# Kernel tuning notes

Measured on AMD Instinct MI355X. Metric: run time of the kernel, lower is better.

The kernel has to match this reference:

```python
import jax, jax.numpy as jnp
import numpy as np

D_MODEL = 512
SEQ_LEN = 2048
S = 32  # local window size
BATCH = 2


def setup_inputs() -> dict:
    key = jax.random.key(0)
    ks = jax.random.split(key, 12)
    shp = (SEQ_LEN, BATCH, D_MODEL)
    return {
        "query": jax.random.normal(ks[0], shp, jnp.float32),
        "key": jax.random.normal(ks[1], shp, jnp.float32),
        "value": jax.random.normal(ks[2], shp, jnp.float32),
        "Wq": jax.random.normal(ks[3], (D_MODEL, D_MODEL), jnp.float32) * 0.02,
        "bq": jax.random.normal(ks[4], (D_MODEL,), jnp.float32) * 0.01,
        "Wk": jax.random.normal(ks[5], (D_MODEL, D_MODEL), jnp.float32) * 0.02,
        "bk": jax.random.normal(ks[6], (D_MODEL,), jnp.float32) * 0.01,
        "Wv": jax.random.normal(ks[7], (D_MODEL, D_MODEL), jnp.float32) * 0.02,
        "bv": jax.random.normal(ks[8], (D_MODEL,), jnp.float32) * 0.01,
        "pos_bias": jax.random.normal(ks[9], (SEQ_LEN, SEQ_LEN), jnp.float32) * 0.02,
        "Wo": jax.random.normal(ks[10], (D_MODEL, D_MODEL), jnp.float32) * 0.02,
        "bo": jax.random.normal(ks[11], (D_MODEL,), jnp.float32) * 0.01,
    }


def _aft_local(query, key, value, Wq, bq, Wk, bk, Wv, bv, pos_bias, Wo, bo):
    T, B, D = query.shape
    q = query @ Wq.T + bq  # [T,B,D]
    k = key @ Wk.T + bk
    v = value @ Wv.T + bv
    pb = pos_bias[:T, :T]

    # max_logit: elementwise max of per-dim key max and (key + col-max of pos_bias) max,
    # then batch index 0 (faithful to original `[0]` indexing) -> shape [D]
    max_logit = jnp.maximum(k.max(axis=0),
                            (k + pb.max(axis=0)[:, None, None]).max(axis=0))[0]

    # out-of-window running sums: tokens t' <= t - S contribute exp(k) (no pos bias)
    ek = jnp.exp(k - max_logit)                 # [T,B,D]
    cs_num = jnp.cumsum(ek * v, axis=0)
    cs_den = jnp.cumsum(ek, axis=0)
    t_arr = jnp.arange(T)
    prefix_idx = jnp.clip(t_arr - S, 0, T - 1)
    has_prefix = (t_arr >= S)[:, None, None]
    num_out = jnp.where(has_prefix, cs_num[prefix_idx], 0.0)
    den_out = jnp.where(has_prefix, cs_den[prefix_idx], 0.0)

    # in-window part: t' in [max(0, t-S+1), t] with pos_bias[t, t']
    j = jnp.arange(S)
    idx_raw = t_arr[:, None] - S + 1 + j[None, :]   # [T,S]
    valid = (idx_raw >= 0).astype(k.dtype)
    idx = jnp.clip(idx_raw, 0, T - 1)
    k_win = k[idx]                                  # [T,S,B,D]
    v_win = v[idx]                                  # [T,S,B,D]
    pb_win = pb[t_arr[:, None], idx]                # [T,S]
    exp_l = jnp.exp(k_win + pb_win[:, :, None, None] - max_logit) * valid[:, :, None, None]
    num_in = (exp_l * v_win).sum(axis=1)            # [T,B,D]
    den_in = exp_l.sum(axis=1)

    y = jax.nn.sigmoid(q) * (num_out + num_in) / (den_out + den_in)
    return y @ Wo.T + bo


def reference(query, key, value, Wq, bq, Wk, bk, Wv, bv, pos_bias, Wo, bo):
    return _aft_local(query, key, value, Wq, bq, Wk, bk, Wv, bv, pos_bias, Wo, bo)
```

## Files before the change

### kernel.cpp

```cpp
#include <hip/hip_runtime.h>
#include <hip/hip_bf16.h>

#define TT 2048
#define BB 2
#define DD 512
#define BD (BB*DD)
#define SS 32
#define MR (TT*BB)
#define NE (TT*BB*DD)
#define CH 32

typedef __bf16 bf16x8 __attribute__((ext_vector_type(8)));
typedef float f32x4 __attribute__((ext_vector_type(4)));

__device__ __forceinline__ void async_copy16(void* lds, const void* gptr) {
    __builtin_amdgcn_global_load_lds(
        (const __attribute__((address_space(1))) void*)gptr,
        (__attribute__((address_space(3))) void*)lds,
        16, 0, 0);
}

__global__ __launch_bounds__(256) void cast_all(
    const float* __restrict__ s0, const float* __restrict__ s1, const float* __restrict__ s2,
    const float* __restrict__ w0, const float* __restrict__ w1,
    const float* __restrict__ w2, const float* __restrict__ w3,
    __hip_bfloat16* __restrict__ d0, __hip_bfloat16* __restrict__ d1, __hip_bfloat16* __restrict__ d2,
    __hip_bfloat16* __restrict__ e0, __hip_bfloat16* __restrict__ e1,
    __hip_bfloat16* __restrict__ e2, __hip_bfloat16* __restrict__ e3)
{
    int b = blockIdx.x;
    const float* s;
    __hip_bfloat16* d;
    size_t i;
    if (b < 6144) {
        int which = b >> 11;
        s = which == 0 ? s0 : (which == 1 ? s1 : s2);
        d = which == 0 ? d0 : (which == 1 ? d1 : d2);
        i = ((size_t)(b & 2047) * 256 + threadIdx.x) * 4;
    } else {
        int b2 = b - 6144;
        int which = b2 >> 8;
        s = which == 0 ? w0 : (which == 1 ? w1 : (which == 2 ? w2 : w3));
        d = which == 0 ? e0 : (which == 1 ? e1 : (which == 2 ? e2 : e3));
        i = ((size_t)(b2 & 255) * 256 + threadIdx.x) * 4;
    }
    float4 f = *(const float4*)(s + i);
    union { __hip_bfloat16 h[4]; ushort4 u; } cv;
    cv.h[0] = __float2bfloat16(f.x); cv.h[1] = __float2bfloat16(f.y);
    cv.h[2] = __float2bfloat16(f.z); cv.h[3] = __float2bfloat16(f.w);
    *(ushort4*)((unsigned short*)d + i) = cv.u;
}

__global__ __launch_bounds__(256) void gemm_qkv(
    const __hip_bfloat16* __restrict__ qb, const __hip_bfloat16* __restrict__ kb,
    const __hip_bfloat16* __restrict__ vb,
    const __hip_bfloat16* __restrict__ Wqb, const __hip_bfloat16* __restrict__ Wkb,
    const __hip_bfloat16* __restrict__ Wvb,
    const float* __restrict__ bq, const float* __restrict__ bk,
    const float* __restrict__ bv,
    float* __restrict__ qout, float* __restrict__ ek, float* __restrict__ ekv,
    float* __restrict__ part_d, float* __restrict__ part_n)
{
    __shared__ char smem[16384];
    const int tid = threadIdx.x;
    const int lane = tid & 63;
    const int wv = tid >> 6;
    const int wave_m = wv >> 1, wave_n = wv & 1;
    const int m0 = blockIdx.y * 64, n0 = blockIdx.x * 64;
    const int kq = lane >> 4, rr = lane & 15;

    if (blockIdx.z == 0) {
        f32x4 acc[2][2] = {};
        const __hip_bfloat16* Arow = qb + (size_t)(m0 + lane) * DD + wv * 8;
        const __hip_bfloat16* Wrow = Wqb + (size_t)(n0 + lane) * DD + wv * 8;
        char* ldsA = &smem[wv * 1024];
        char* ldsW = &smem[4096 + wv * 1024];
        for (int k0 = 0; k0 < DD; k0 += 32) {
            __syncthreads();
            async_copy16(ldsA, Arow + k0);
            async_copy16(ldsW, Wrow + k0);
            __syncthreads();
            bf16x8 a0 = *(const bf16x8*)&smem[kq*1024 + (wave_m*32 +  0 + rr)*16];
            bf16x8 a1 = *(const bf16x8*)&smem[kq*1024 + (wave_m*32 + 16 + rr)*16];
            bf16x8 b0 = *(const bf16x8*)&smem[4096 + kq*1024 + (wave_n*32 +  0 + rr)*16];
            bf16x8 b1 = *(const bf16x8*)&smem[4096 + kq*1024 + (wave_n*32 + 16 + rr)*16];
            acc[0][0] = __builtin_amdgcn_mfma_f32_16x16x32_bf16(a0, b0, acc[0][0], 0, 0, 0);
            acc[0][1] = __builtin_amdgcn_mfma_f32_16x16x32_bf16(a0, b1, acc[0][1], 0, 0, 0);
            acc[1][0] = __builtin_amdgcn_mfma_f32_16x16x32_bf16(a1, b0, acc[1][0], 0, 0, 0);
            acc[1][1] = __builtin_amdgcn_mfma_f32_16x16x32_bf16(a1, b1, acc[1][1], 0, 0, 0);
        }
        #pragma unroll
        for (int ms = 0; ms < 2; ++ms)
            #pragma unroll
            for (int ns = 0; ns < 2; ++ns) {
                int n = n0 + wave_n*32 + ns*16 + rr;
                float bn = bq[n];
                #pragma unroll
                for (int r = 0; r < 4; ++r) {
                    int m = m0 + wave_m*32 + ms*16 + kq*4 + r;
                    qout[(size_t)m * DD + n] = acc[ms][ns][r] + bn;
                }
            }
    } else {
        f32x4 acck[2][2] = {}, accv[2][2] = {};
        const __hip_bfloat16* AKrow = kb + (size_t)(m0 + lane) * DD + wv * 8;
        const __hip_bfloat16* WKrow = Wkb + (size_t)(n0 + lane) * DD + wv * 8;
        const __hip_bfloat16* AVrow = vb + (size_t)(m0 + lane) * DD + wv * 8;
        const __hip_bfloat16* WVrow = Wvb + (size_t)(n0 + lane) * DD + wv * 8;
        char* ldsAK = &smem[wv * 1024];
        char* ldsWK = &smem[4096 + wv * 1024];
        char* ldsAV = &smem[8192 + wv * 1024];
        char* ldsWV = &smem[12288 + wv * 1024];
        for (int k0 = 0; k0 < DD; k0 += 32) {
            __syncthreads();
            async_copy16(ldsAK, AKrow + k0);
            async_copy16(ldsWK, WKrow + k0);
            async_copy16(ldsAV, AVrow + k0);
            async_copy16(ldsWV, WVrow + k0);
            __syncthreads();
            bf16x8 ak0 = *(const bf16x8*)&smem[kq*1024 + (wave_m*32 +  0 + rr)*16];
            bf16x8 ak1 = *(const bf16x8*)&smem[kq*1024 + (wave_m*32 + 16 + rr)*16];
            bf16x8 bk0 = *(const bf16x8*)&smem[4096 + kq*1024 + (wave_n*32 +  0 + rr)*16];
            bf16x8 bk1 = *(const bf16x8*)&smem[4096 + kq*1024 + (wave_n*32 + 16 + rr)*16];
            bf16x8 av0 = *(const bf16x8*)&smem[8192 + kq*1024 + (wave_m*32 +  0 + rr)*16];
            bf16x8 av1 = *(const bf16x8*)&smem[8192 + kq*1024 + (wave_m*32 + 16 + rr)*16];
            bf16x8 bv0 = *(const bf16x8*)&smem[12288 + kq*1024 + (wave_n*32 +  0 + rr)*16];
            bf16x8 bv1 = *(const bf16x8*)&smem[12288 + kq*1024 + (wave_n*32 + 16 + rr)*16];
            acck[0][0] = __builtin_amdgcn_mfma_f32_16x16x32_bf16(ak0, bk0, acck[0][0], 0, 0, 0);
            acck[0][1] = __builtin_amdgcn_mfma_f32_16x16x32_bf16(ak0, bk1, acck[0][1], 0, 0, 0);
            acck[1][0] = __builtin_amdgcn_mfma_f32_16x16x32_bf16(ak1, bk0, acck[1][0], 0, 0, 0);
            acck[1][1] = __builtin_amdgcn_mfma_f32_16x16x32_bf16(ak1, bk1, acck[1][1], 0, 0, 0);
            accv[0][0] = __builtin_amdgcn_mfma_f32_16x16x32_bf16(av0, bv0, accv[0][0], 0, 0, 0);
            accv[0][1] = __builtin_amdgcn_mfma_f32_16x16x32_bf16(av0, bv1, accv[0][1], 0, 0, 0);
            accv[1][0] = __builtin_amdgcn_mfma_f32_16x16x32_bf16(av1, bv0, accv[1][0], 0, 0, 0);
            accv[1][1] = __builtin_amdgcn_mfma_f32_16x16x32_bf16(av1, bv1, accv[1][1], 0, 0, 0);
        }
        float sd[2][2] = {{0.f,0.f},{0.f,0.f}};
        float sn[2][2] = {{0.f,0.f},{0.f,0.f}};
        #pragma unroll
        for (int ms = 0; ms < 2; ++ms)
            #pragma unroll
            for (int ns = 0; ns < 2; ++ns) {
                int n = n0 + wave_n*32 + ns*16 + rr;
                float bkn = bk[n], bvn = bv[n];
                #pragma unroll
                for (int r = 0; r < 4; ++r) {
                    int m = m0 + wave_m*32 + ms*16 + kq*4 + r;
                    float e  = expf(acck[ms][ns][r] + bkn);
                    float nv = e * (accv[ms][ns][r] + bvn);
                    ek[(size_t)m * DD + n]  = e;
                    ekv[(size_t)m * DD + n] = nv;
                    sd[ns][r & 1] += e;
                    sn[ns][r & 1] += nv;
                }
            }
        #pragma unroll
        for (int ns = 0; ns < 2; ++ns)
            #pragma unroll
            for (int par = 0; par < 2; ++par) {
                sd[ns][par] += __shfl_xor(sd[ns][par], 16, 64);
                sd[ns][par] += __shfl_xor(sd[ns][par], 32, 64);
                sn[ns][par] += __shfl_xor(sn[ns][par], 16, 64);
                sn[ns][par] += __shfl_xor(sn[ns][par], 32, 64);
            }
        __syncthreads();
        float* red = (float*)smem;
        if (lane < 16) {
            #pragma unroll
            for (int ns = 0; ns < 2; ++ns) {
                int c = wave_n*32 + ns*16 + rr;
                red[(0*2 + wave_m)*64 + c] = sd[ns][0];
                red[(1*2 + wave_m)*64 + c] = sd[ns][1];
                red[(2*2 + wave_m)*64 + c] = sn[ns][0];
                red[(3*2 + wave_m)*64 + c] = sn[ns][1];
            }
        }
        __syncthreads();
        {
            int which = tid >> 6;
            int c = tid & 63;
            float s = red[(which*2 + 0)*64 + c] + red[(which*2 + 1)*64 + c];
            int b = which & 1;
            float* dst = (which < 2) ? part_d : part_n;
            dst[(size_t)blockIdx.y * BD + b*512 + n0 + c] = s;
        }
    }
}

__global__ __launch_bounds__(256) void fused_window(
    const float* __restrict__ q, const float* __restrict__ ek,
    const float* __restrict__ ekv, const float* __restrict__ part_d,
    const float* __restrict__ part_n, const float* __restrict__ pb,
    __hip_bfloat16* __restrict__ yb)
{
    __shared__ float wl[CH][SS];
    const int tid = threadIdx.x;
    const int col = blockIdx.x * 256 + tid;
    const int chunk = blockIdx.y;
    const int t0 = chunk * CH;

    #pragma unroll
    for (int i = 0; i < (CH * SS) / 256; ++i) {
        int idx = tid + i * 256;
        int tl = idx >> 5, j = idx & 31;
        int t = t0 + tl;
        int u = t - (SS - 1) + j;
        float w = 0.f;
        if (u >= 0) w = expf(pb[(size_t)t * TT + u]);
        wl[tl][j] = w;
    }
    __syncthreads();

    float ring_d[32], ring_n[32];
    float cs_d = 0.f, cs_n = 0.f;
    const bool hasp = (chunk > 0);
    if (hasp) {
        float pref_d = 0.f, pref_n = 0.f;
        for (int p = 0; p < chunk; ++p) {
            pref_d += part_d[(size_t)p * BD + col];
            pref_n += part_n[(size_t)p * BD + col];
        }
        float ssd = 0.f, ssn = 0.f;
        #pragma unroll
        for (int i = 0; i < 32; ++i) {
            size_t off = (size_t)(t0 - 32 + i) * BD + col;
            float e = ek[off];
            float n = ekv[off];
            ring_d[i] = e; ring_n[i] = n;
            ssd += e; ssn += n;
        }
        cs_d = pref_d - ssd;
        cs_n = pref_n - ssn;
    } else {
        #pragma unroll
        for (int i = 0; i < 32; ++i) { ring_d[i] = 0.f; ring_n[i] = 0.f; }
    }

    #pragma unroll
    for (int s = 0; s < CH; ++s) {
        int t = t0 + s;
        size_t off = (size_t)t * BD + col;
        float e = ek[off];
        float n = ekv[off];
        cs_d += ring_d[s];
        cs_n += ring_n[s];
        ring_d[s] = e;
        ring_n[s] = n;
        float den = 0.f, num = 0.f;
        #pragma unroll
        for (int j4 = 0; j4 < 8; ++j4) {
            float4 w4 = *(const float4*)&wl[s][j4 * 4];
            den += w4.x * ring_d[(s + 1 + j4*4 + 0) & 31];
            num += w4.x * ring_n[(s + 1 + j4*4 + 0) & 31];
            den += w4.y * ring_d[(s + 1 + j4*4 + 1) & 31];
            num += w4.y * ring_n[(s + 1 + j4*4 + 1) & 31];
            den += w4.z * ring_d[(s + 1 + j4*4 + 2) & 31];
            num += w4.z * ring_n[(s + 1 + j4*4 + 2) & 31];
            den += w4.w * ring_d[(s + 1 + j4*4 + 3) & 31];
            num += w4.w * ring_n[(s + 1 + j4*4 + 3) & 31];
        }
        if (hasp) { den += cs_d; num += cs_n; }
        float qv = q[off];
        float sig = 1.f / (1.f + expf(-qv));
        yb[off] = __float2bfloat16(sig * num / den);
    }
}

__global__ __launch_bounds__(256) void gemm_out(
    const __hip_bfloat16* __restrict__ yb, const __hip_bfloat16* __restrict__ Wob,
    const float* __restrict__ bo, float* __restrict__ out)
{
    __shared__ char smem[8192];
    const int tid = threadIdx.x;
    const int lane = tid & 63;
    const int wv = tid >> 6;
    const int wave_m = wv >> 1, wave_n = wv & 1;
    const int m0 = blockIdx.y * 64, n0 = blockIdx.x * 64;
    const int kq = lane >> 4, rr = lane & 15;

    f32x4 acc[2][2] = {};
    const __hip_bfloat16* Arow = yb + (size_t)(m0 + lane) * DD + wv * 8;
    const __hip_bfloat16* Wrow = Wob + (size_t)(n0 + lane) * DD + wv * 8;
    char* ldsA = &smem[wv * 1024];
    char* ldsW = &smem[4096 + wv * 1024];

    for (int k0 = 0; k0 < DD; k0 += 32) {
        __syncthreads();
        async_copy16(ldsA, Arow + k0);
        async_copy16(ldsW, Wrow + k0);
        __syncthreads();
        bf16x8 a0 = *(const bf16x8*)&smem[kq*1024 + (wave_m*32 +  0 + rr)*16];
        bf16x8 a1 = *(const bf16x8*)&smem[kq*1024 + (wave_m*32 + 16 + rr)*16];
        bf16x8 b0 = *(const bf16x8*)&smem[4096 + kq*1024 + (wave_n*32 +  0 + rr)*16];
        bf16x8 b1 = *(const bf16x8*)&smem[4096 + kq*1024 + (wave_n*32 + 16 + rr)*16];
        acc[0][0] = __builtin_amdgcn_mfma_f32_16x16x32_bf16(a0, b0, acc[0][0], 0, 0, 0);
        acc[0][1] = __builtin_amdgcn_mfma_f32_16x16x32_bf16(a0, b1, acc[0][1], 0, 0, 0);
        acc[1][0] = __builtin_amdgcn_mfma_f32_16x16x32_bf16(a1, b0, acc[1][0], 0, 0, 0);
        acc[1][1] = __builtin_amdgcn_mfma_f32_16x16x32_bf16(a1, b1, acc[1][1], 0, 0, 0);
    }
    #pragma unroll
    for (int ms = 0; ms < 2; ++ms)
        #pragma unroll
        for (int ns = 0; ns < 2; ++ns) {
            int n = n0 + wave_n*32 + ns*16 + rr;
            float bn = bo[n];
            #pragma unroll
            for (int r = 0; r < 4; ++r) {
                int m = m0 + wave_m*32 + ms*16 + kq*4 + r;
                out[(size_t)m * DD + n] = acc[ms][ns][r] + bn;
            }
        }
}

extern "C" void kernel_launch(void* const* d_in, const int* in_sizes, int n_in,
                              void* d_out, int out_size, void* d_ws, size_t ws_size,
                              hipStream_t stream) {
    const float* query = (const float*)d_in[0];
    const float* key   = (const float*)d_in[1];
    const float* value = (const float*)d_in[2];
    const float* Wq    = (const float*)d_in[3];
    const float* bq    = (const float*)d_in[4];
    const float* Wk    = (const float*)d_in[5];
    const float* bk    = (const float*)d_in[6];
    const float* Wv    = (const float*)d_in[7];
    const float* bv    = (const float*)d_in[8];
    const float* pb    = (const float*)d_in[9];
    const float* Wo    = (const float*)d_in[10];
    const float* bo    = (const float*)d_in[11];
    float* out = (float*)d_out;

    float* ws = (float*)d_ws;
    float* q      = ws;
    float* ek     = ws + (size_t)NE;
    float* ekv    = ws + (size_t)2 * NE;
    float* part_d = ws + (size_t)3 * NE;
    float* part_n = part_d + 65536;
    __hip_bfloat16* bfb = (__hip_bfloat16*)(part_n + 65536);
    __hip_bfloat16* qb  = bfb;
    __hip_bfloat16* kb  = bfb + (size_t)NE;
    __hip_bfloat16* vb  = bfb + (size_t)2 * NE;
    __hip_bfloat16* yb  = bfb + (size_t)3 * NE;
    __hip_bfloat16* Wqb = bfb + (size_t)4 * NE;
    __hip_bfloat16* Wkb = Wqb + 262144;
    __hip_bfloat16* Wvb = Wkb + 262144;
    __hip_bfloat16* Wob = Wvb + 262144;

    cast_all<<<7168, 256, 0, stream>>>(query, key, value, Wq, Wk, Wv, Wo,
                                       qb, kb, vb, Wqb, Wkb, Wvb, Wob);

    gemm_qkv<<<dim3(DD / 64, MR / 64, 2), 256, 0, stream>>>(
        qb, kb, vb, Wqb, Wkb, Wvb, bq, bk, bv,
        q, ek, ekv, part_d, part_n);

    fused_window<<<dim3(BD / 256, TT / CH), 256, 0, stream>>>(
        q, ek, ekv, part_d, part_n, pb, yb);

    gemm_out<<<dim3(DD / 64, MR / 64), 256, 0, stream>>>(yb, Wob, bo, out);
}
```

Measured before the change: 174.8 us.

## Triple-buffer GEMM K-loops with async LDS prefetch and interleave ek/ekv storage

Replaces the load-then-compute loops in the QKV and output GEMMs with a three-stage LDS ring. Tiles are prefetched two iterations ahead using explicit vmcnt waits and raw barriers, so global-to-LDS copies overlap MFMA work. It also interleaves the ek/ekv outputs and the per-chunk partial sums into float2 pairs, so the window kernel issues one vector load instead of two scalar loads. The prefix-sum loop uses four independent accumulators. LDS use per block grows threefold, which may reduce occupancy, and the hand-written waitcnt logic must count outstanding copies correctly.

```diff
diff --git a/kernel.cpp b/kernel.cpp
--- a/kernel.cpp
+++ b/kernel.cpp
@@ -19,6 +19,8 @@
         (__attribute__((address_space(3))) void*)lds,
         16, 0, 0);
 }
+
+#define MFMA16(a,b,c) __builtin_amdgcn_mfma_f32_16x16x32_bf16((a),(b),(c),0,0,0)
 
 __global__ __launch_bounds__(256) void cast_all(
     const float* __restrict__ s0, const float* __restrict__ s1, const float* __restrict__ s2,
@@ -58,10 +60,10 @@
     const __hip_bfloat16* __restrict__ Wvb,
     const float* __restrict__ bq, const float* __restrict__ bk,
     const float* __restrict__ bv,
-    float* __restrict__ qout, float* __restrict__ ek, float* __restrict__ ekv,
-    float* __restrict__ part_d, float* __restrict__ part_n)
+    float* __restrict__ qout, float* __restrict__ ekn,
+    float* __restrict__ part)
 {
-    __shared__ char smem[16384];
+    __shared__ char smem[49152];
     const int tid = threadIdx.x;
     const int lane = tid & 63;
     const int wv = tid >> 6;
@@ -73,21 +75,33 @@
         f32x4 acc[2][2] = {};
         const __hip_bfloat16* Arow = qb + (size_t)(m0 + lane) * DD + wv * 8;
         const __hip_bfloat16* Wrow = Wqb + (size_t)(n0 + lane) * DD + wv * 8;
-        char* ldsA = &smem[wv * 1024];
-        char* ldsW = &smem[4096 + wv * 1024];
-        for (int k0 = 0; k0 < DD; k0 += 32) {
-            __syncthreads();
-            async_copy16(ldsA, Arow + k0);
-            async_copy16(ldsW, Wrow + k0);
-            __syncthreads();
-            bf16x8 a0 = *(const bf16x8*)&smem[kq*1024 + (wave_m*32 +  0 + rr)*16];
-            bf16x8 a1 = *(const bf16x8*)&smem[kq*1024 + (wave_m*32 + 16 + rr)*16];
-            bf16x8 b0 = *(const bf16x8*)&smem[4096 + kq*1024 + (wave_n*32 +  0 + rr)*16];
-            bf16x8 b1 = *(const bf16x8*)&smem[4096 + kq*1024 + (wave_n*32 + 16 + rr)*16];
-            acc[0][0] = __builtin_amdgcn_mfma_f32_16x16x32_bf16(a0, b0, acc[0][0], 0, 0, 0);
-            acc[0][1] = __builtin_amdgcn_mfma_f32_16x16x32_bf16(a0, b1, acc[0][1], 0, 0, 0);
-            acc[1][0] = __builtin_amdgcn_mfma_f32_16x16x32_bf16(a1, b0, acc[1][0], 0, 0, 0);
-            acc[1][1] = __builtin_amdgcn_mfma_f32_16x16x32_bf16(a1, b1, acc[1][1], 0, 0, 0);
+        async_copy16(smem + 0*8192 +        wv*1024, Arow + 0);
+        async_copy16(smem + 0*8192 + 4096 + wv*1024, Wrow + 0);
+        async_copy16(smem + 1*8192 +        wv*1024, Arow + 32);
+        async_copy16(smem + 1*8192 + 4096 + wv*1024, Wrow + 32);
+        asm volatile("s_waitcnt vmcnt(2)" ::: "memory");
+        __builtin_amdgcn_s_barrier();
+        #pragma unroll
+        for (int it = 0; it < 16; ++it) {
+            if (it + 2 < 16) {
+                char* nb = smem + ((it + 2) % 3) * 8192;
+                async_copy16(nb +        wv*1024, Arow + (it+2)*32);
+                async_copy16(nb + 4096 + wv*1024, Wrow + (it+2)*32);
+            }
+            const char* cb = smem + (it % 3) * 8192;
+            bf16x8 a0 = *(const bf16x8*)(cb + kq*1024 + (wave_m*32 +  0 + rr)*16);
+            bf16x8 a1 = *(const bf16x8*)(cb + kq*1024 + (wave_m*32 + 16 + rr)*16);
+            bf16x8 w0 = *(const bf16x8*)(cb + 4096 + kq*1024 + (wave_n*32 +  0 + rr)*16);
+            bf16x8 w1 = *(const bf16x8*)(cb + 4096 + kq*1024 + (wave_n*32 + 16 + rr)*16);
+            acc[0][0] = MFMA16(a0, w0, acc[0][0]);
+            acc[0][1] = MFMA16(a0, w1, acc[0][1]);
+            acc[1][0] = MFMA16(a1, w0, acc[1][0]);
+            acc[1][1] = MFMA16(a1, w1, acc[1][1]);
+            if (it < 15) {
+                if (it < 14) asm volatile("s_waitcnt vmcnt(2) lgkmcnt(0)" ::: "memory");
+                else         asm volatile("s_waitcnt vmcnt(0) lgkmcnt(0)" ::: "memory");
+                __builtin_amdgcn_s_barrier();
+            }
         }
         #pragma unroll
         for (int ms = 0; ms < 2; ++ms)
@@ -107,33 +121,47 @@
         const __hip_bfloat16* WKrow = Wkb + (size_t)(n0 + lane) * DD + wv * 8;
         const __hip_bfloat16* AVrow = vb + (size_t)(m0 + lane) * DD + wv * 8;
         const __hip_bfloat16* WVrow = Wvb + (size_t)(n0 + lane) * DD + wv * 8;
-        char* ldsAK = &smem[wv * 1024];
-        char* ldsWK = &smem[4096 + wv * 1024];
-        char* ldsAV = &smem[8192 + wv * 1024];
-        char* ldsWV = &smem[12288 + wv * 1024];
-        for (int k0 = 0; k0 < DD; k0 += 32) {
-            __syncthreads();
-            async_copy16(ldsAK, AKrow + k0);
-            async_copy16(ldsWK, WKrow + k0);
-            async_copy16(ldsAV, AVrow + k0);
-            async_copy16(ldsWV, WVrow + k0);
-            __syncthreads();
-            bf16x8 ak0 = *(const bf16x8*)&smem[kq*1024 + (wave_m*32 +  0 + rr)*16];
-            bf16x8 ak1 = *(const bf16x8*)&smem[kq*1024 + (wave_m*32 + 16 + rr)*16];
-            bf16x8 bk0 = *(const bf16x8*)&smem[4096 + kq*1024 + (wave_n*32 +  0 + rr)*16];
-            bf16x8 bk1 = *(const bf16x8*)&smem[4096 + kq*1024 + (wave_n*32 + 16 + rr)*16];
-            bf16x8 av0 = *(const bf16x8*)&smem[8192 + kq*1024 + (wave_m*32 +  0 + rr)*16];
-            bf16x8 av1 = *(const bf16x8*)&smem[8192 + kq*1024 + (wave_m*32 + 16 + rr)*16];
-            bf16x8 bv0 = *(const bf16x8*)&smem[12288 + kq*1024 + (wave_n*32 +  0 + rr)*16];
-            bf16x8 bv1 = *(const bf16x8*)&smem[12288 + kq*1024 + (wave_n*32 + 16 + rr)*16];
-            acck[0][0] = __builtin_amdgcn_mfma_f32_16x16x32_bf16(ak0, bk0, acck[0][0], 0, 0, 0);
-            acck[0][1] = __builtin_amdgcn_mfma_f32_16x16x32_bf16(ak0, bk1, acck[0][1], 0, 0, 0);
-            acck[1][0] = __builtin_amdgcn_mfma_f32_16x16x32_bf16(ak1, bk0, acck[1][0], 0, 0, 0);
-            acck[1][1] = __builtin_amdgcn_mfma_f32_16x16x32_bf16(ak1, bk1, acck[1][1], 0, 0, 0);
-            accv[0][0] = __builtin_amdgcn_mfma_f32_16x16x32_bf16(av0, bv0, accv[0][0], 0, 0, 0);
-            accv[0][1] = __builtin_amdgcn_mfma_f32_16x16x32_bf16(av0, bv1, accv[0][1], 0, 0, 0);
-            accv[1][0] = __builtin_amdgcn_mfma_f32_16x16x32_bf16(av1, bv0, accv[1][0], 0, 0, 0);
-            accv[1][1] = __builtin_amdgcn_mfma_f32_16x16x32_bf16(av1, bv1, accv[1][1], 0, 0, 0);
+        #pragma unroll
+        for (int pt = 0; pt < 2; ++pt) {
+            char* nb = smem + pt * 16384;
+            async_copy16(nb +         wv*1024, AKrow + pt*32);
+            async_copy16(nb +  4096 + wv*1024, WKrow + pt*32);
+            async_copy16(nb +  8192 + wv*1024, AVrow + pt*32);
+            async_copy16(nb + 12288 + wv*1024, WVrow + pt*32);
+        }
+        asm volatile("s_waitcnt vmcnt(4)" ::: "memory");
+        __builtin_amdgcn_s_barrier();
+        #pragma unroll
+        for (int it = 0; it < 16; ++it) {
+            if (it + 2 < 16) {
+                char* nb = smem + ((it + 2) % 3) * 16384;
+                async_copy16(nb +         wv*1024, AKrow + (it+2)*32);
+                async_copy16(nb +  4096 + wv*1024, WKrow + (it+2)*32);
+                async_copy16(nb +  8192 + wv*1024, AVrow + (it+2)*32);
+                async_copy16(nb + 12288 + wv*1024, WVrow + (it+2)*32);
+            }
+            const char* cb = smem + (it % 3) * 16384;
+            bf16x8 ak0 = *(const bf16x8*)(cb +         kq*1024 + (wave_m*32 +  0 + rr)*16);
+            bf16x8 ak1 = *(const bf16x8*)(cb +         kq*1024 + (wave_m*32 + 16 + rr)*16);
+            bf16x8 bk0 = *(const bf16x8*)(cb +  4096 + kq*1024 + (wave_n*32 +  0 + rr)*16);
+            bf16x8 bk1 = *(const bf16x8*)(cb +  4096 + kq*1024 + (wave_n*32 + 16 + rr)*16);
+            bf16x8 av0 = *(const bf16x8*)(cb +  8192 + kq*1024 + (wave_m*32 +  0 + rr)*16);
+            bf16x8 av1 = *(const bf16x8*)(cb +  8192 + kq*1024 + (wave_m*32 + 16 + rr)*16);
+            bf16x8 bv0 = *(const bf16x8*)(cb + 12288 + kq*1024 + (wave_n*32 +  0 + rr)*16);
+            bf16x8 bv1 = *(const bf16x8*)(cb + 12288 + kq*1024 + (wave_n*32 + 16 + rr)*16);
+            acck[0][0] = MFMA16(ak0, bk0, acck[0][0]);
+            acck[0][1] = MFMA16(ak0, bk1, acck[0][1]);
+            acck[1][0] = MFMA16(ak1, bk0, acck[1][0]);
+            acck[1][1] = MFMA16(ak1, bk1, acck[1][1]);
+            accv[0][0] = MFMA16(av0, bv0, accv[0][0]);
+            accv[0][1] = MFMA16(av0, bv1, accv[0][1]);
+            accv[1][0] = MFMA16(av1, bv0, accv[1][0]);
+            accv[1][1] = MFMA16(av1, bv1, accv[1][1]);
+            if (it < 15) {
+                if (it < 14) asm volatile("s_waitcnt vmcnt(4) lgkmcnt(0)" ::: "memory");
+                else         asm volatile("s_waitcnt vmcnt(0) lgkmcnt(0)" ::: "memory");
+                __builtin_amdgcn_s_barrier();
+            }
         }
         float sd[2][2] = {{0.f,0.f},{0.f,0.f}};
         float sn[2][2] = {{0.f,0.f},{0.f,0.f}};
@@ -148,8 +176,8 @@
                     int m = m0 + wave_m*32 + ms*16 + kq*4 + r;
                     float e  = expf(acck[ms][ns][r] + bkn);
                     float nv = e * (accv[ms][ns][r] + bvn);
-                    ek[(size_t)m * DD + n]  = e;
-                    ekv[(size_t)m * DD + n] = nv;
+                    float2 st; st.x = e; st.y = nv;
+                    *(float2*)&ekn[((size_t)m * DD + n) * 2] = st;
                     sd[ns][r & 1] += e;
                     sn[ns][r & 1] += nv;
                 }
@@ -181,16 +209,15 @@
             int c = tid & 63;
             float s = red[(which*2 + 0)*64 + c] + red[(which*2 + 1)*64 + c];
             int b = which & 1;
-            float* dst = (which < 2) ? part_d : part_n;
-            dst[(size_t)blockIdx.y * BD + b*512 + n0 + c] = s;
+            int sel = which >> 1;
+            part[((size_t)blockIdx.y * BD + b*512 + n0 + c) * 2 + sel] = s;
         }
     }
 }
 
 __global__ __launch_bounds__(256) void fused_window(
-    const float* __restrict__ q, const float* __restrict__ ek,
-    const float* __restrict__ ekv, const float* __restrict__ part_d,
-    const float* __restrict__ part_n, const float* __restrict__ pb,
+    const float* __restrict__ q, const float* __restrict__ ekn,
+    const float* __restrict__ part, const float* __restrict__ pb,
     __hip_bfloat16* __restrict__ yb)
 {
     __shared__ float wl[CH][SS];
@@ -215,19 +242,27 @@
     float cs_d = 0.f, cs_n = 0.f;
     const bool hasp = (chunk > 0);
     if (hasp) {
-        float pref_d = 0.f, pref_n = 0.f;
-        for (int p = 0; p < chunk; ++p) {
-            pref_d += part_d[(size_t)p * BD + col];
-            pref_n += part_n[(size_t)p * BD + col];
-        }
+        float pd[4] = {0.f,0.f,0.f,0.f}, pn[4] = {0.f,0.f,0.f,0.f};
+        int p = 0;
+        for (; p + 4 <= chunk; p += 4) {
+            #pragma unroll
+            for (int u2 = 0; u2 < 4; ++u2) {
+                float2 v = *(const float2*)&part[((size_t)(p + u2) * BD + col) * 2];
+                pd[u2] += v.x; pn[u2] += v.y;
+            }
+        }
+        for (; p < chunk; ++p) {
+            float2 v = *(const float2*)&part[((size_t)p * BD + col) * 2];
+            pd[0] += v.x; pn[0] += v.y;
+        }
+        float pref_d = (pd[0] + pd[1]) + (pd[2] + pd[3]);
+        float pref_n = (pn[0] + pn[1]) + (pn[2] + pn[3]);
         float ssd = 0.f, ssn = 0.f;
         #pragma unroll
         for (int i = 0; i < 32; ++i) {
-            size_t off = (size_t)(t0 - 32 + i) * BD + col;
-            float e = ek[off];
-            float n = ekv[off];
-            ring_d[i] = e; ring_n[i] = n;
-            ssd += e; ssn += n;
+            float2 v = *(const float2*)&ekn[((size_t)(t0 - 32 + i) * BD + col) * 2];
+            ring_d[i] = v.x; ring_n[i] = v.y;
+            ssd += v.x; ssn += v.y;
         }
         cs_d = pref_d - ssd;
         cs_n = pref_n - ssn;
@@ -240,12 +275,11 @@
     for (int s = 0; s < CH; ++s) {
         int t = t0 + s;
         size_t off = (size_t)t * BD + col;
-        float e = ek[off];
-        float n = ekv[off];
+        float2 env = *(const float2*)&ekn[off * 2];
         cs_d += ring_d[s];
         cs_n += ring_n[s];
-        ring_d[s] = e;
-        ring_n[s] = n;
+        ring_d[s] = env.x;
+        ring_n[s] = env.y;
         float den = 0.f, num = 0.f;
         #pragma unroll
         for (int j4 = 0; j4 < 8; ++j4) {
@@ -270,7 +304,7 @@
     const __hip_bfloat16* __restrict__ yb, const __hip_bfloat16* __restrict__ Wob,
     const float* __restrict__ bo, float* __restrict__ out)
 {
-    __shared__ char smem[8192];
+    __shared__ char smem[24576];
     const int tid = threadIdx.x;
     const int lane = tid & 63;
     const int wv = tid >> 6;
@@ -281,22 +315,34 @@
     f32x4 acc[2][2] = {};
     const __hip_bfloat16* Arow = yb + (size_t)(m0 + lane) * DD + wv * 8;
     const __hip_bfloat16* Wrow = Wob + (size_t)(n0 + lane) * DD + wv * 8;
-    char* ldsA = &smem[wv * 1024];
-    char* ldsW = &smem[4096 + wv * 1024];
-
-    for (int k0 = 0; k0 < DD; k0 += 32) {
-        __syncthreads();
-        async_copy16(ldsA, Arow + k0);
-        async_copy16(ldsW, Wrow + k0);
-        __syncthreads();
-        bf16x8 a0 = *(const bf16x8*)&smem[kq*1024 + (wave_m*32 +  0 + rr)*16];
-        bf16x8 a1 = *(const bf16x8*)&smem[kq*1024 + (wave_m*32 + 16 + rr)*16];
-        bf16x8 b0 = *(const bf16x8*)&smem[4096 + kq*1024 + (wave_n*32 +  0 + rr)*16];
-        bf16x8 b1 = *(const bf16x8*)&smem[4096 + kq*1024 + (wave_n*32 + 16 + rr)*16];
-        acc[0][0] = __builtin_amdgcn_mfma_f32_16x16x32_bf16(a0, b0, acc[0][0], 0, 0, 0);
-        acc[0][1] = __builtin_amdgcn_mfma_f32_16x16x32_bf16(a0, b1, acc[0][1], 0, 0, 0);
-        acc[1][0] = __builtin_amdgcn_mfma_f32_16x16x32_bf16(a1, b0, acc[1][0], 0, 0, 0);
-        acc[1][1] = __builtin_amdgcn_mfma_f32_16x16x32_bf16(a1, b1, acc[1][1], 0, 0, 0);
+
+    async_copy16(smem + 0*8192 +        wv*1024, Arow + 0);
+    async_copy16(smem + 0*8192 + 4096 + wv*1024, Wrow + 0);
+    async_copy16(smem + 1*8192 +        wv*1024, Arow + 32);
+    async_copy16(smem + 1*8192 + 4096 + wv*1024, Wrow + 32);
+    asm volatile("s_waitcnt vmcnt(2)" ::: "memory");
+    __builtin_amdgcn_s_barrier();
+    #pragma unroll
+    for (int it = 0; it < 16; ++it) {
+        if (it + 2 < 16) {
+            char* nb = smem + ((it + 2) % 3) * 8192;
+            async_copy16(nb +        wv*1024, Arow + (it+2)*32);
+            async_copy16(nb + 4096 + wv*1024, Wrow + (it+2)*32);
+        }
+        const char* cb = smem + (it % 3) * 8192;
+        bf16x8 a0 = *(const bf16x8*)(cb + kq*1024 + (wave_m*32 +  0 + rr)*16);
+        bf16x8 a1 = *(const bf16x8*)(cb + kq*1024 + (wave_m*32 + 16 + rr)*16);
+        bf16x8 w0 = *(const bf16x8*)(cb + 4096 + kq*1024 + (wave_n*32 +  0 + rr)*16);
+        bf16x8 w1 = *(const bf16x8*)(cb + 4096 + kq*1024 + (wave_n*32 + 16 + rr)*16);
+        acc[0][0] = MFMA16(a0, w0, acc[0][0]);
+        acc[0][1] = MFMA16(a0, w1, acc[0][1]);
+        acc[1][0] = MFMA16(a1, w0, acc[1][0]);
+        acc[1][1] = MFMA16(a1, w1, acc[1][1]);
+        if (it < 15) {
+            if (it < 14) asm volatile("s_waitcnt vmcnt(2) lgkmcnt(0)" ::: "memory");
+            else         asm volatile("s_waitcnt vmcnt(0) lgkmcnt(0)" ::: "memory");
+            __builtin_amdgcn_s_barrier();
+        }
     }
     #pragma unroll
     for (int ms = 0; ms < 2; ++ms)
@@ -330,12 +376,10 @@
     float* out = (float*)d_out;
 
     float* ws = (float*)d_ws;
-    float* q      = ws;
-    float* ek     = ws + (size_t)NE;
-    float* ekv    = ws + (size_t)2 * NE;
-    float* part_d = ws + (size_t)3 * NE;
-    float* part_n = part_d + 65536;
-    __hip_bfloat16* bfb = (__hip_bfloat16*)(part_n + 65536);
+    float* q    = ws;
+    float* ekn  = ws + (size_t)NE;
+    float* part = ws + (size_t)3 * NE;
+    __hip_bfloat16* bfb = (__hip_bfloat16*)(part + 131072);
     __hip_bfloat16* qb  = bfb;
     __hip_bfloat16* kb  = bfb + (size_t)NE;
     __hip_bfloat16* vb  = bfb + (size_t)2 * NE;
@@ -350,10 +394,10 @@
 
     gemm_qkv<<<dim3(DD / 64, MR / 64, 2), 256, 0, stream>>>(
         qb, kb, vb, Wqb, Wkb, Wvb, bq, bk, bv,
-        q, ek, ekv, part_d, part_n);
+        q, ekn, part);
 
     fused_window<<<dim3(BD / 256, TT / CH), 256, 0, stream>>>(
-        q, ek, ekv, part_d, part_n, pb, yb);
+        q, ekn, part, pb, yb);
 
     gemm_out<<<dim3(DD / 64, MR / 64), 256, 0, stream>>>(yb, Wob, bo, out);
 }
```

Measured after the change: 172.0 us. About the same (-1.6%).
